# Optimization experiments

Hardware: AMD Instinct MI355X
Metric: run time of the kernel (lower is better)

## Reference

```python
import jax, jax.numpy as jnp
import numpy as np

B, V = 256, 128000

def setup_inputs() -> dict:
    key = jax.random.key(0)
    k1, k2, k3 = jax.random.split(key, 3)
    logits = jax.random.normal(k1, (B, V), dtype=jnp.float32)
    # temperatures in [0,1); force a few exact zeros to exercise the greedy path
    temperatures = jax.random.uniform(k2, (B,), dtype=jnp.float32)
    temperatures = temperatures.at[:8].set(0.0)
    # uniform noise for Gumbel-max sampling (stand-in for torch.multinomial RNG)
    uniform_noise = jax.random.uniform(k3, (B, V), dtype=jnp.float32,
                                       minval=1e-7, maxval=1.0 - 1e-7)
    return {"logits": logits, "temperatures": temperatures, "uniform_noise": uniform_noise}

def reference(logits, temperatures, uniform_noise):
    logits = logits.astype(jnp.float32)
    greedy_tokens = jnp.argmax(logits, axis=-1)                     # [B]
    safe_t = jnp.where(temperatures == 0, jnp.ones_like(temperatures), temperatures)
    scaled = logits / safe_t[:, None]                               # [B, V]
    probs = jax.nn.softmax(scaled, axis=-1)                         # [B, V]
    # Gumbel-max trick: argmax(scaled + g), g ~ Gumbel(0,1) == multinomial(probs)
    gumbel = -jnp.log(-jnp.log(uniform_noise))
    sample_tokens = jnp.argmax(scaled + gumbel, axis=-1)            # [B]
    tokens = jnp.where(temperatures == 0, greedy_tokens, sample_tokens)
    return tokens, probs
```

## Files before the change

### kernel.cpp

```cpp
#include <hip/hip_runtime.h>
#include <math.h>

#define BATCH 256
#define VOCAB 128000
#define V4 (VOCAB / 4)
#define NTHREADS 1024
#define NWAVES (NTHREADS / 64)

typedef float vfloat4 __attribute__((ext_vector_type(4)));

__global__ __launch_bounds__(NTHREADS) void sampler_kernel(
    const float* __restrict__ logits,
    const float* __restrict__ temps,
    const float* __restrict__ noise,
    float* __restrict__ out_tokens,
    float* __restrict__ out_probs)
{
    const int b   = blockIdx.x;
    const int tid = threadIdx.x;
    const int wave = tid >> 6;
    const int lane = tid & 63;

    const float t      = temps[b];
    const float safe_t = (t == 0.0f) ? 1.0f : t;
    const float inv_t  = 1.0f / safe_t;

    const vfloat4* lg4 = (const vfloat4*)(logits + (size_t)b * VOCAB);
    const vfloat4* nz4 = (const vfloat4*)(noise  + (size_t)b * VOCAB);
    vfloat4*       pb4 = (vfloat4*)(out_probs + (size_t)b * VOCAB);

    float m = -INFINITY, s = 0.0f;
    float gv = -INFINITY; int gi = 0;

    for (int i = tid; i < V4; i += NTHREADS) {
        vfloat4 x4 = lg4[i];
#pragma unroll
        for (int j = 0; j < 4; ++j) {
            const int   idx = 4 * i + j;
            const float x   = x4[j];
            const float sc  = x * inv_t;
            if (x > gv) { gv = x; gi = idx; }
            const float mn = fmaxf(m, sc);
            s = s * __expf(m - mn) + __expf(sc - mn);
            m = mn;
        }
    }

#pragma unroll
    for (int off = 32; off >= 1; off >>= 1) {
        float m2  = __shfl_down(m,  off);
        float s2  = __shfl_down(s,  off);
        float gv2 = __shfl_down(gv, off);
        int   gi2 = __shfl_down(gi, off);
        float mn = fmaxf(m, m2);
        s = s * __expf(m - mn) + s2 * __expf(m2 - mn);
        m = mn;
        if (gv2 > gv || (gv2 == gv && gi2 < gi)) { gv = gv2; gi = gi2; }
    }

    __shared__ float sm[NWAVES], ss[NWAVES], sgv[NWAVES];
    __shared__ int   sgi[NWAVES];
    __shared__ float bM, binvS;
    __shared__ int   bGI;
    if (lane == 0) { sm[wave] = m; ss[wave] = s; sgv[wave] = gv; sgi[wave] = gi; }
    __syncthreads();
    if (tid == 0) {
        float M = sm[0], S = ss[0], GV = sgv[0]; int GI = sgi[0];
        for (int w = 1; w < NWAVES; ++w) {
            float mn = fmaxf(M, sm[w]);
            S = S * __expf(M - mn) + ss[w] * __expf(sm[w] - mn);
            M = mn;
            if (sgv[w] > GV || (sgv[w] == GV && sgi[w] < GI)) { GV = sgv[w]; GI = sgi[w]; }
        }
        bM = M; binvS = 1.0f / S; bGI = GI;
    }
    __syncthreads();
    const float M    = bM;
    const float invS = binvS;

    float sv = -INFINITY; int si = 0;

    for (int i = tid; i < V4; i += NTHREADS) {
        vfloat4 x4 = lg4[i];
        vfloat4 u4 = __builtin_nontemporal_load(&nz4[i]);
        vfloat4 p;
#pragma unroll
        for (int j = 0; j < 4; ++j) {
            const int   idx = 4 * i + j;
            const float sc  = x4[j] * inv_t;
            p[j] = __expf(sc - M) * invS;
            const float g = -__logf(-__logf(u4[j]));
            const float z = sc + g;
            if (z > sv) { sv = z; si = idx; }
        }
        __builtin_nontemporal_store(p, &pb4[i]);
    }

#pragma unroll
    for (int off = 32; off >= 1; off >>= 1) {
        float sv2 = __shfl_down(sv, off);
        int   si2 = __shfl_down(si, off);
        if (sv2 > sv || (sv2 == sv && si2 < si)) { sv = sv2; si = si2; }
    }
    __shared__ float ssv[NWAVES];
    __shared__ int   ssi[NWAVES];
    if (lane == 0) { ssv[wave] = sv; ssi[wave] = si; }
    __syncthreads();
    if (tid == 0) {
        float SV = ssv[0]; int SI = ssi[0];
        for (int w = 1; w < NWAVES; ++w) {
            if (ssv[w] > SV || (ssv[w] == SV && ssi[w] < SI)) { SV = ssv[w]; SI = ssi[w]; }
        }
        const int token = (t == 0.0f) ? bGI : SI;
        out_tokens[b] = (float)token;
    }
}

extern "C" void kernel_launch(void* const* d_in, const int* in_sizes, int n_in,
                              void* d_out, int out_size, void* d_ws, size_t ws_size,
                              hipStream_t stream) {
    const float* logits = (const float*)d_in[0];
    const float* temps  = (const float*)d_in[1];
    const float* noise  = (const float*)d_in[2];
    float* out = (float*)d_out;
    sampler_kernel<<<BATCH, NTHREADS, 0, stream>>>(logits, temps, noise,
                                                   out, out + BATCH);
}
```

Before: 318.5 us.

## Split row reduction across blocks with partial/combine/probs kernels

Replaces the one-block-per-row sampler with three kernels. The first computes per-chunk max, exp-sum, greedy argmax and Gumbel argmax over 25 parts per row, holding the data in registers. A small combine kernel merges the partials into tokens and softmax stats, and a third kernel writes the normalized probabilities. This spreads each row over many more blocks, since 256 large blocks underfill the GPU. It also folds the Gumbel argmax into the first pass and replaces the online softmax with a max-then-sum over registers. In exchange it adds two extra launches, a workspace round trip and a second read of the logits.

```diff
diff --git a/kernel.cpp b/kernel.cpp
--- a/kernel.cpp
+++ b/kernel.cpp
@@ -1,118 +1,187 @@
 #include <hip/hip_runtime.h>
 #include <math.h>
+#include <limits.h>
 
 #define BATCH 256
 #define VOCAB 128000
-#define V4 (VOCAB / 4)
-#define NTHREADS 1024
-#define NWAVES (NTHREADS / 64)
+#define ROW_V4 (VOCAB / 4)
+#define PARTS 25
+#define PART_V4 (ROW_V4 / PARTS)
+#define ATHREADS 256
+#define PER_THREAD (PART_V4 / ATHREADS)
+#define AWAVES (ATHREADS / 64)
 
 typedef float vfloat4 __attribute__((ext_vector_type(4)));
 
-__global__ __launch_bounds__(NTHREADS) void sampler_kernel(
+#define WS_PARTIALS_FLOATS (BATCH * PARTS * 8)
+
+__global__ __launch_bounds__(ATHREADS) void partial_kernel(
     const float* __restrict__ logits,
     const float* __restrict__ temps,
     const float* __restrict__ noise,
+    float* __restrict__ ws_partials)
+{
+    const int part = blockIdx.x;
+    const int row  = blockIdx.y;
+    const int tid  = threadIdx.x;
+    const int wave = tid >> 6;
+    const int lane = tid & 63;
+
+    const float t     = temps[row];
+    const float inv_t = (t == 0.0f) ? 1.0f : (1.0f / t);
+
+    const vfloat4* lg4 = (const vfloat4*)(logits + (size_t)row * VOCAB);
+    const vfloat4* nz4 = (const vfloat4*)(noise  + (size_t)row * VOCAB);
+    const int base = part * PART_V4 + tid;
+
+    vfloat4 x[PER_THREAD], u[PER_THREAD];
+#pragma unroll
+    for (int k = 0; k < PER_THREAD; ++k) x[k] = lg4[base + k * ATHREADS];
+#pragma unroll
+    for (int k = 0; k < PER_THREAD; ++k)
+        u[k] = __builtin_nontemporal_load(&nz4[base + k * ATHREADS]);
+
+    float mx = -INFINITY;
+    float gv = -INFINITY; int gi = 0;
+    float zv = -INFINITY; int zi = 0;
+#pragma unroll
+    for (int k = 0; k < PER_THREAD; ++k) {
+#pragma unroll
+        for (int j = 0; j < 4; ++j) {
+            const int   idx = (base + k * ATHREADS) * 4 + j;
+            const float xx  = x[k][j];
+            mx = fmaxf(mx, xx);
+            if (xx > gv) { gv = xx; gi = idx; }
+            const float g = -__logf(-__logf(u[k][j]));
+            const float z = __fmaf_rn(xx, inv_t, g);
+            if (z > zv) { zv = z; zi = idx; }
+        }
+    }
+
+#pragma unroll
+    for (int off = 32; off >= 1; off >>= 1) {
+        mx = fmaxf(mx, __shfl_down(mx, off));
+        float gv2 = __shfl_down(gv, off); int gi2 = __shfl_down(gi, off);
+        if (gv2 > gv || (gv2 == gv && gi2 < gi)) { gv = gv2; gi = gi2; }
+        float zv2 = __shfl_down(zv, off); int zi2 = __shfl_down(zi, off);
+        if (zv2 > zv || (zv2 == zv && zi2 < zi)) { zv = zv2; zi = zi2; }
+    }
+
+    __shared__ float smx[AWAVES], sgv[AWAVES], szv[AWAVES];
+    __shared__ int   sgi[AWAVES], szi[AWAVES];
+    __shared__ float bMx;
+    if (lane == 0) { smx[wave] = mx; sgv[wave] = gv; sgi[wave] = gi;
+                     szv[wave] = zv; szi[wave] = zi; }
+    __syncthreads();
+    if (tid == 0) {
+        float M = smx[0];
+        for (int w = 1; w < AWAVES; ++w) M = fmaxf(M, smx[w]);
+        bMx = M;
+    }
+    __syncthreads();
+    const float Mx = bMx;
+
+    float s0 = 0.f, s1 = 0.f, s2 = 0.f, s3 = 0.f;
+#pragma unroll
+    for (int k = 0; k < PER_THREAD; ++k) {
+        s0 += __expf((x[k][0] - Mx) * inv_t);
+        s1 += __expf((x[k][1] - Mx) * inv_t);
+        s2 += __expf((x[k][2] - Mx) * inv_t);
+        s3 += __expf((x[k][3] - Mx) * inv_t);
+    }
+    float ps = (s0 + s1) + (s2 + s3);
+#pragma unroll
+    for (int off = 32; off >= 1; off >>= 1) ps += __shfl_down(ps, off);
+
+    __shared__ float ssum[AWAVES];
+    if (lane == 0) ssum[wave] = ps;
+    __syncthreads();
+    if (tid == 0) {
+        float S = 0.f;
+        for (int w = 0; w < AWAVES; ++w) S += ssum[w];
+        float GV = sgv[0]; int GI = sgi[0];
+        float ZV = szv[0]; int ZI = szi[0];
+        for (int w = 1; w < AWAVES; ++w) {
+            if (sgv[w] > GV || (sgv[w] == GV && sgi[w] < GI)) { GV = sgv[w]; GI = sgi[w]; }
+            if (szv[w] > ZV || (szv[w] == ZV && szi[w] < ZI)) { ZV = szv[w]; ZI = szi[w]; }
+        }
+        float* rec = ws_partials + ((size_t)row * PARTS + part) * 8;
+        rec[0] = Mx; rec[1] = S; rec[2] = GV; ((int*)rec)[3] = GI;
+        rec[4] = ZV; ((int*)rec)[5] = ZI;
+    }
+}
+
+__global__ __launch_bounds__(64) void combine_kernel(
+    const float* __restrict__ temps,
+    const float* __restrict__ ws_partials,
     float* __restrict__ out_tokens,
+    float* __restrict__ ws_row)
+{
+    const int row  = blockIdx.x;
+    const int lane = threadIdx.x;
+
+    const float t     = temps[row];
+    const float inv_t = (t == 0.0f) ? 1.0f : (1.0f / t);
+
+    float Mxp = -INFINITY, Sp = 0.f;
+    float gv = -INFINITY; int gi = INT_MAX;
+    float zv = -INFINITY; int zi = INT_MAX;
+    if (lane < PARTS) {
+        const float* rec = ws_partials + ((size_t)row * PARTS + lane) * 8;
+        Mxp = rec[0]; Sp = rec[1];
+        gv = rec[2]; gi = ((const int*)rec)[3];
+        zv = rec[4]; zi = ((const int*)rec)[5];
+    }
+    float Mx = Mxp;
+#pragma unroll
+    for (int off = 32; off >= 1; off >>= 1) Mx = fmaxf(Mx, __shfl_xor(Mx, off));
+
+    float s = (lane < PARTS) ? Sp * __expf((Mxp - Mx) * inv_t) : 0.f;
+#pragma unroll
+    for (int off = 32; off >= 1; off >>= 1) {
+        s += __shfl_xor(s, off);
+        float gv2 = __shfl_xor(gv, off); int gi2 = __shfl_xor(gi, off);
+        if (gv2 > gv || (gv2 == gv && gi2 < gi)) { gv = gv2; gi = gi2; }
+        float zv2 = __shfl_xor(zv, off); int zi2 = __shfl_xor(zi, off);
+        if (zv2 > zv || (zv2 == zv && zi2 < zi)) { zv = zv2; zi = zi2; }
+    }
+    if (lane == 0) {
+        const int token = (t == 0.0f) ? gi : zi;
+        out_tokens[row] = (float)token;
+        ws_row[row * 2 + 0] = Mx * inv_t;
+        ws_row[row * 2 + 1] = 1.0f / s;
+    }
+}
+
+__global__ __launch_bounds__(ATHREADS) void probs_kernel(
+    const float* __restrict__ logits,
+    const float* __restrict__ temps,
+    const float* __restrict__ ws_row,
     float* __restrict__ out_probs)
 {
-    const int b   = blockIdx.x;
-    const int tid = threadIdx.x;
-    const int wave = tid >> 6;
-    const int lane = tid & 63;
-
-    const float t      = temps[b];
-    const float safe_t = (t == 0.0f) ? 1.0f : t;
-    const float inv_t  = 1.0f / safe_t;
-
-    const vfloat4* lg4 = (const vfloat4*)(logits + (size_t)b * VOCAB);
-    const vfloat4* nz4 = (const vfloat4*)(noise  + (size_t)b * VOCAB);
-    vfloat4*       pb4 = (vfloat4*)(out_probs + (size_t)b * VOCAB);
-
-    float m = -INFINITY, s = 0.0f;
-    float gv = -INFINITY; int gi = 0;
-
-    for (int i = tid; i < V4; i += NTHREADS) {
-        vfloat4 x4 = lg4[i];
-#pragma unroll
-        for (int j = 0; j < 4; ++j) {
-            const int   idx = 4 * i + j;
-            const float x   = x4[j];
-            const float sc  = x * inv_t;
-            if (x > gv) { gv = x; gi = idx; }
-            const float mn = fmaxf(m, sc);
-            s = s * __expf(m - mn) + __expf(sc - mn);
-            m = mn;
-        }
-    }
-
-#pragma unroll
-    for (int off = 32; off >= 1; off >>= 1) {
-        float m2  = __shfl_down(m,  off);
-        float s2  = __shfl_down(s,  off);
-        float gv2 = __shfl_down(gv, off);
-        int   gi2 = __shfl_down(gi, off);
-        float mn = fmaxf(m, m2);
-        s = s * __expf(m - mn) + s2 * __expf(m2 - mn);
-        m = mn;
-        if (gv2 > gv || (gv2 == gv && gi2 < gi)) { gv = gv2; gi = gi2; }
-    }
-
-    __shared__ float sm[NWAVES], ss[NWAVES], sgv[NWAVES];
-    __shared__ int   sgi[NWAVES];
-    __shared__ float bM, binvS;
-    __shared__ int   bGI;
-    if (lane == 0) { sm[wave] = m; ss[wave] = s; sgv[wave] = gv; sgi[wave] = gi; }
-    __syncthreads();
-    if (tid == 0) {
-        float M = sm[0], S = ss[0], GV = sgv[0]; int GI = sgi[0];
-        for (int w = 1; w < NWAVES; ++w) {
-            float mn = fmaxf(M, sm[w]);
-            S = S * __expf(M - mn) + ss[w] * __expf(sm[w] - mn);
-            M = mn;
-            if (sgv[w] > GV || (sgv[w] == GV && sgi[w] < GI)) { GV = sgv[w]; GI = sgi[w]; }
-        }
-        bM = M; binvS = 1.0f / S; bGI = GI;
-    }
-    __syncthreads();
-    const float M    = bM;
-    const float invS = binvS;
-
-    float sv = -INFINITY; int si = 0;
-
-    for (int i = tid; i < V4; i += NTHREADS) {
-        vfloat4 x4 = lg4[i];
-        vfloat4 u4 = __builtin_nontemporal_load(&nz4[i]);
+    const int part = blockIdx.x;
+    const int row  = blockIdx.y;
+    const int tid  = threadIdx.x;
+
+    const float t     = temps[row];
+    const float inv_t = (t == 0.0f) ? 1.0f : (1.0f / t);
+    const float Msc   = ws_row[row * 2 + 0];
+    const float invS  = ws_row[row * 2 + 1];
+
+    const vfloat4* lg4 = (const vfloat4*)(logits + (size_t)row * VOCAB);
+    vfloat4*       pb4 = (vfloat4*)(out_probs + (size_t)row * VOCAB);
+    const int base = part * PART_V4 + tid;
+
+    vfloat4 x[PER_THREAD];
+#pragma unroll
+    for (int k = 0; k < PER_THREAD; ++k) x[k] = lg4[base + k * ATHREADS];
+#pragma unroll
+    for (int k = 0; k < PER_THREAD; ++k) {
         vfloat4 p;
 #pragma unroll
-        for (int j = 0; j < 4; ++j) {
-            const int   idx = 4 * i + j;
-            const float sc  = x4[j] * inv_t;
-            p[j] = __expf(sc - M) * invS;
-            const float g = -__logf(-__logf(u4[j]));
-            const float z = sc + g;
-            if (z > sv) { sv = z; si = idx; }
-        }
-        __builtin_nontemporal_store(p, &pb4[i]);
-    }
-
-#pragma unroll
-    for (int off = 32; off >= 1; off >>= 1) {
-        float sv2 = __shfl_down(sv, off);
-        int   si2 = __shfl_down(si, off);
-        if (sv2 > sv || (sv2 == sv && si2 < si)) { sv = sv2; si = si2; }
-    }
-    __shared__ float ssv[NWAVES];
-    __shared__ int   ssi[NWAVES];
-    if (lane == 0) { ssv[wave] = sv; ssi[wave] = si; }
-    __syncthreads();
-    if (tid == 0) {
-        float SV = ssv[0]; int SI = ssi[0];
-        for (int w = 1; w < NWAVES; ++w) {
-            if (ssv[w] > SV || (ssv[w] == SV && ssi[w] < SI)) { SV = ssv[w]; SI = ssi[w]; }
-        }
-        const int token = (t == 0.0f) ? bGI : SI;
-        out_tokens[b] = (float)token;
+        for (int j = 0; j < 4; ++j)
+            p[j] = __expf(__fmaf_rn(x[k][j], inv_t, -Msc)) * invS;
+        __builtin_nontemporal_store(p, &pb4[base + k * ATHREADS]);
     }
 }
 
@@ -123,6 +192,13 @@
     const float* temps  = (const float*)d_in[1];
     const float* noise  = (const float*)d_in[2];
     float* out = (float*)d_out;
-    sampler_kernel<<<BATCH, NTHREADS, 0, stream>>>(logits, temps, noise,
-                                                   out, out + BATCH);
-}
+    float* ws_partials = (float*)d_ws;
+    float* ws_row      = ws_partials + WS_PARTIALS_FLOATS;
+
+    partial_kernel<<<dim3(PARTS, BATCH), ATHREADS, 0, stream>>>(
+        logits, temps, noise, ws_partials);
+    combine_kernel<<<BATCH, 64, 0, stream>>>(
+        temps, ws_partials, out, ws_row);
+    probs_kernel<<<dim3(PARTS, BATCH), ATHREADS, 0, stream>>>(
+        logits, temps, ws_row, out + BATCH);
+}
```

Measured after the change: 323.5 us. No clear change (+1.6%).
